# Performance work log

Hardware: AMD Instinct MI355X
Metric: run time of the kernel (lower is better)

The kernel has to match this reference:

```python
import jax, jax.numpy as jnp
import numpy as np

B, T, I, H = 8192, 1024, 3, 4


def setup_inputs() -> dict:
    key = jax.random.key(0)
    k_x, k_wi, k_wh, k_bi, k_bh = jax.random.split(key, 5)
    s = 1.0 / np.sqrt(H)  # PyTorch GRU init scale uniform(-1/sqrt(H), 1/sqrt(H))
    return {
        "x": jax.random.normal(k_x, (B, T, I), dtype=jnp.float32),
        "w_ih": jax.random.uniform(k_wi, (3 * H, I), jnp.float32, -s, s),
        "w_hh": jax.random.uniform(k_wh, (3 * H, H), jnp.float32, -s, s),
        "b_ih": jax.random.uniform(k_bi, (3 * H,), jnp.float32, -s, s),
        "b_hh": jax.random.uniform(k_bh, (3 * H,), jnp.float32, -s, s),
    }


def _gru_forward(x, w_ih, w_hh, b_ih, b_hh):
    # Precompute input projections for all timesteps: [B, T, 3H]
    gi = jnp.einsum('bti,gi->btg', x, w_ih) + b_ih
    gi = jnp.swapaxes(gi, 0, 1)  # [T, B, 3H] for scan over time
    h0 = jnp.zeros((x.shape[0], H), dtype=x.dtype)

    def step(h, gi_t):
        gh = h @ w_hh.T + b_hh                      # [B, 3H]
        i_r, i_z, i_n = jnp.split(gi_t, 3, axis=-1)
        h_r, h_z, h_n = jnp.split(gh, 3, axis=-1)
        r = jax.nn.sigmoid(i_r + h_r)
        z = jax.nn.sigmoid(i_z + h_z)
        n = jnp.tanh(i_n + r * h_n)
        h_new = (1.0 - z) * n + z * h
        return h_new, h_new

    h_last, outs = jax.lax.scan(step, h0, gi)
    out = jnp.swapaxes(outs, 0, 1)  # [B, T, H] (batch_first)
    h_n = h_last[None]              # [1, B, H] (num_layers*dirs, B, H)
    return out, h_n


def reference(x, w_ih, w_hh, b_ih, b_hh):
    return _gru_forward(x, w_ih, w_hh, b_ih, b_hh)
```

## Files before the change

kernel.cpp:

```cpp
#include <hip/hip_runtime.h>


#define TC 32
#define XS_STRIDE 99
#define OS_STRIDE 132

template<int CTRL>
__device__ __forceinline__ float dpp_rot(float v) {
    int i = __builtin_bit_cast(int, v);
    int r = __builtin_amdgcn_mov_dpp(i, CTRL, 0xf, 0xf, true);
    return __builtin_bit_cast(float, r);
}

__device__ __forceinline__ float vrcp(float x) { return __builtin_amdgcn_rcpf(x); }

__device__ __forceinline__ float sigmoid_f(float x) {
    return vrcp(1.0f + __expf(-x));
}
__device__ __forceinline__ float tanh_f(float x) {
    float e = __expf(2.0f * x);
    return 1.0f - 2.0f * vrcp(e + 1.0f);
}

__global__ __launch_bounds__(64) void gru_kernel(
    const float* __restrict__ x,
    const float* __restrict__ w_ih,
    const float* __restrict__ w_hh,
    const float* __restrict__ b_ih,
    const float* __restrict__ b_hh,
    float* __restrict__ out)
{
    __shared__ float x_s[16 * XS_STRIDE];
    __shared__ float out_s[16 * OS_STRIDE];

    const int lane = threadIdx.x;
    const int bl   = lane >> 2;
    const int j    = lane & 3;
    const int b0   = blockIdx.x * 16;

    float wir[3], wiz[3], win[3];
    #pragma unroll
    for (int k = 0; k < 3; ++k) {
        wir[k] = w_ih[j * 3 + k];
        wiz[k] = w_ih[(4 + j) * 3 + k];
        win[k] = w_ih[(8 + j) * 3 + k];
    }
    float whr[4], whz[4], whn[4];
    #pragma unroll
    for (int m = 0; m < 4; ++m) {
        int k = (j + m) & 3;
        whr[m] = w_hh[j * 4 + k];
        whz[m] = w_hh[(4 + j) * 4 + k];
        whn[m] = w_hh[(8 + j) * 4 + k];
    }
    const float br  = b_ih[j]     + b_hh[j];
    const float bz  = b_ih[4 + j] + b_hh[4 + j];
    const float bin = b_ih[8 + j];
    const float bhn = b_hh[8 + j];

    float h = 0.0f;

    float4 xr[6];
    {
        #pragma unroll
        for (int u = 0; u < 6; ++u) {
            int f  = u * 64 + lane;
            int bb = f / 24;
            int q  = f - bb * 24;
            xr[u] = *(const float4*)(x + (long long)(b0 + bb) * 3072 + q * 4);
        }
    }

    for (int c = 0; c < 32; ++c) {
        #pragma unroll
        for (int u = 0; u < 6; ++u) {
            int f  = u * 64 + lane;
            int bb = f / 24;
            int q  = f - bb * 24;
            float* p = &x_s[bb * XS_STRIDE + q * 4];
            p[0] = xr[u].x; p[1] = xr[u].y; p[2] = xr[u].z; p[3] = xr[u].w;
        }
        __syncthreads();

        if (c < 31) {
            int t0 = (c + 1) * TC;
            #pragma unroll
            for (int u = 0; u < 6; ++u) {
                int f  = u * 64 + lane;
                int bb = f / 24;
                int q  = f - bb * 24;
                xr[u] = *(const float4*)(x + (long long)(b0 + bb) * 3072 + t0 * 3 + q * 4);
            }
        }

        const float* xs = &x_s[bl * XS_STRIDE];
        float*       os = &out_s[bl * OS_STRIDE];
        #pragma unroll 8
        for (int t = 0; t < TC; ++t) {
            float x0 = xs[t * 3 + 0], x1 = xs[t * 3 + 1], x2 = xs[t * 3 + 2];
            float sr = fmaf(wir[0], x0, fmaf(wir[1], x1, fmaf(wir[2], x2, br)));
            float sz = fmaf(wiz[0], x0, fmaf(wiz[1], x1, fmaf(wiz[2], x2, bz)));
            float sn = fmaf(win[0], x0, fmaf(win[1], x1, fmaf(win[2], x2, bin)));

            float h1 = dpp_rot<0x39>(h);
            float h2 = dpp_rot<0x4E>(h);
            float h3 = dpp_rot<0x93>(h);

            float gr = fmaf(whr[0], h, fmaf(whr[1], h1, fmaf(whr[2], h2, whr[3] * h3)));
            float gz = fmaf(whz[0], h, fmaf(whz[1], h1, fmaf(whz[2], h2, whz[3] * h3)));
            float gn = fmaf(whn[0], h, fmaf(whn[1], h1, fmaf(whn[2], h2, whn[3] * h3)));

            float r = sigmoid_f(sr + gr);
            float z = sigmoid_f(sz + gz);
            float n = tanh_f(fmaf(r, gn + bhn, sn));
            h = fmaf(z, h - n, n);

            os[t * 4 + j] = h;
        }
        __syncthreads();

        int t0 = c * TC;
        #pragma unroll
        for (int u = 0; u < 8; ++u) {
            int f  = u * 64 + lane;
            int bb = f >> 5;
            int q  = f & 31;
            float4 v = *(const float4*)&out_s[bb * OS_STRIDE + q * 4];
            *(float4*)(out + (long long)(b0 + bb) * 4096 + t0 * 4 + q * 4) = v;
        }
    }

    out[33554432LL + (long long)(b0 + bl) * 4 + j] = h;
}

extern "C" void kernel_launch(void* const* d_in, const int* in_sizes, int n_in,
                              void* d_out, int out_size, void* d_ws, size_t ws_size,
                              hipStream_t stream) {
    const float* x    = (const float*)d_in[0];
    const float* w_ih = (const float*)d_in[1];
    const float* w_hh = (const float*)d_in[2];
    const float* b_ih = (const float*)d_in[3];
    const float* b_hh = (const float*)d_in[4];
    float* out = (float*)d_out;

    dim3 grid(512), block(64);
    gru_kernel<<<grid, block, 0, stream>>>(x, w_ih, w_hh, b_ih, b_hh, out);
}
```

Before: 278.6 us.

## Interleave two batch recurrences per wave and fold log2e into weights

Each 64-lane block now processes 32 batch rows instead of 16. Every lane advances two independent GRU chains interleaved per timestep, exposing instruction-level parallelism in the serial recurrence. Weights and biases are pre-scaled by -log2(e) or 2·log2(e) so the gate activations use raw exp2 and reciprocal with no extra multiplies. The grid is halved to 256 blocks, which may leave SIMDs idle and increase register and LDS use per block.

```diff
diff --git a/kernel.cpp b/kernel.cpp
--- a/kernel.cpp
+++ b/kernel.cpp
@@ -12,15 +12,8 @@
     return __builtin_bit_cast(float, r);
 }
 
-__device__ __forceinline__ float vrcp(float x) { return __builtin_amdgcn_rcpf(x); }
-
-__device__ __forceinline__ float sigmoid_f(float x) {
-    return vrcp(1.0f + __expf(-x));
-}
-__device__ __forceinline__ float tanh_f(float x) {
-    float e = __expf(2.0f * x);
-    return 1.0f - 2.0f * vrcp(e + 1.0f);
-}
+__device__ __forceinline__ float vrcp(float x)  { return __builtin_amdgcn_rcpf(x); }
+__device__ __forceinline__ float vexp2(float x) { return __builtin_amdgcn_exp2f(x); }
 
 __global__ __launch_bounds__(64) void gru_kernel(
     const float* __restrict__ x,
@@ -30,54 +23,55 @@
     const float* __restrict__ b_hh,
     float* __restrict__ out)
 {
-    __shared__ float x_s[16 * XS_STRIDE];
-    __shared__ float out_s[16 * OS_STRIDE];
+    __shared__ float x_s[32 * XS_STRIDE];
+    __shared__ float out_s[32 * OS_STRIDE];
 
     const int lane = threadIdx.x;
-    const int bl   = lane >> 2;
+    const int q    = lane >> 2;
     const int j    = lane & 3;
-    const int b0   = blockIdx.x * 16;
+    const int b0   = blockIdx.x * 32;
+
+    const float NL2E = -1.4426950408889634f;
+    const float P2   =  2.8853900817779268f;
 
     float wir[3], wiz[3], win[3];
     #pragma unroll
     for (int k = 0; k < 3; ++k) {
-        wir[k] = w_ih[j * 3 + k];
-        wiz[k] = w_ih[(4 + j) * 3 + k];
-        win[k] = w_ih[(8 + j) * 3 + k];
+        wir[k] = NL2E * w_ih[j * 3 + k];
+        wiz[k] = NL2E * w_ih[(4 + j) * 3 + k];
+        win[k] = P2   * w_ih[(8 + j) * 3 + k];
     }
     float whr[4], whz[4], whn[4];
     #pragma unroll
     for (int m = 0; m < 4; ++m) {
         int k = (j + m) & 3;
-        whr[m] = w_hh[j * 4 + k];
-        whz[m] = w_hh[(4 + j) * 4 + k];
-        whn[m] = w_hh[(8 + j) * 4 + k];
+        whr[m] = NL2E * w_hh[j * 4 + k];
+        whz[m] = NL2E * w_hh[(4 + j) * 4 + k];
+        whn[m] = P2   * w_hh[(8 + j) * 4 + k];
     }
-    const float br  = b_ih[j]     + b_hh[j];
-    const float bz  = b_ih[4 + j] + b_hh[4 + j];
-    const float bin = b_ih[8 + j];
-    const float bhn = b_hh[8 + j];
+    const float br   = NL2E * (b_ih[j]     + b_hh[j]);
+    const float bz   = NL2E * (b_ih[4 + j] + b_hh[4 + j]);
+    const float bin  = P2   * b_ih[8 + j];
+    const float bhn  = P2   * b_hh[8 + j];
 
-    float h = 0.0f;
+    float h[2] = {0.0f, 0.0f};
 
-    float4 xr[6];
-    {
-        #pragma unroll
-        for (int u = 0; u < 6; ++u) {
-            int f  = u * 64 + lane;
-            int bb = f / 24;
-            int q  = f - bb * 24;
-            xr[u] = *(const float4*)(x + (long long)(b0 + bb) * 3072 + q * 4);
-        }
+    float4 xr[12];
+    #pragma unroll
+    for (int u = 0; u < 12; ++u) {
+        int f  = u * 64 + lane;
+        int bb = f / 24;
+        int q4 = f - bb * 24;
+        xr[u] = *(const float4*)(x + (long long)(b0 + bb) * 3072 + q4 * 4);
     }
 
     for (int c = 0; c < 32; ++c) {
         #pragma unroll
-        for (int u = 0; u < 6; ++u) {
+        for (int u = 0; u < 12; ++u) {
             int f  = u * 64 + lane;
             int bb = f / 24;
-            int q  = f - bb * 24;
-            float* p = &x_s[bb * XS_STRIDE + q * 4];
+            int q4 = f - bb * 24;
+            float* p = &x_s[bb * XS_STRIDE + q4 * 4];
             p[0] = xr[u].x; p[1] = xr[u].y; p[2] = xr[u].z; p[3] = xr[u].w;
         }
         __syncthreads();
@@ -85,52 +79,63 @@
         if (c < 31) {
             int t0 = (c + 1) * TC;
             #pragma unroll
-            for (int u = 0; u < 6; ++u) {
+            for (int u = 0; u < 12; ++u) {
                 int f  = u * 64 + lane;
                 int bb = f / 24;
-                int q  = f - bb * 24;
-                xr[u] = *(const float4*)(x + (long long)(b0 + bb) * 3072 + t0 * 3 + q * 4);
+                int q4 = f - bb * 24;
+                xr[u] = *(const float4*)(x + (long long)(b0 + bb) * 3072 + t0 * 3 + q4 * 4);
             }
         }
 
-        const float* xs = &x_s[bl * XS_STRIDE];
-        float*       os = &out_s[bl * OS_STRIDE];
+        const float* xsA = &x_s[q * XS_STRIDE];
+        const float* xsB = &x_s[(q + 16) * XS_STRIDE];
+        float*       osA = &out_s[q * OS_STRIDE];
+        float*       osB = &out_s[(q + 16) * OS_STRIDE];
         #pragma unroll 8
         for (int t = 0; t < TC; ++t) {
-            float x0 = xs[t * 3 + 0], x1 = xs[t * 3 + 1], x2 = xs[t * 3 + 2];
-            float sr = fmaf(wir[0], x0, fmaf(wir[1], x1, fmaf(wir[2], x2, br)));
-            float sz = fmaf(wiz[0], x0, fmaf(wiz[1], x1, fmaf(wiz[2], x2, bz)));
-            float sn = fmaf(win[0], x0, fmaf(win[1], x1, fmaf(win[2], x2, bin)));
+            float x0[2], x1[2], x2[2];
+            x0[0] = xsA[t * 3 + 0]; x1[0] = xsA[t * 3 + 1]; x2[0] = xsA[t * 3 + 2];
+            x0[1] = xsB[t * 3 + 0]; x1[1] = xsB[t * 3 + 1]; x2[1] = xsB[t * 3 + 2];
+            #pragma unroll
+            for (int p = 0; p < 2; ++p) {
+                float sr = fmaf(wir[0], x0[p], fmaf(wir[1], x1[p], fmaf(wir[2], x2[p], br)));
+                float sz = fmaf(wiz[0], x0[p], fmaf(wiz[1], x1[p], fmaf(wiz[2], x2[p], bz)));
+                float sn = fmaf(win[0], x0[p], fmaf(win[1], x1[p], fmaf(win[2], x2[p], bin)));
 
-            float h1 = dpp_rot<0x39>(h);
-            float h2 = dpp_rot<0x4E>(h);
-            float h3 = dpp_rot<0x93>(h);
+                float h1 = dpp_rot<0x39>(h[p]);
+                float h2 = dpp_rot<0x4E>(h[p]);
+                float h3 = dpp_rot<0x93>(h[p]);
 
-            float gr = fmaf(whr[0], h, fmaf(whr[1], h1, fmaf(whr[2], h2, whr[3] * h3)));
-            float gz = fmaf(whz[0], h, fmaf(whz[1], h1, fmaf(whz[2], h2, whz[3] * h3)));
-            float gn = fmaf(whn[0], h, fmaf(whn[1], h1, fmaf(whn[2], h2, whn[3] * h3)));
+                float gr = fmaf(whr[0], h[p], fmaf(whr[1], h1, fmaf(whr[2], h2, whr[3] * h3)));
+                float gz = fmaf(whz[0], h[p], fmaf(whz[1], h1, fmaf(whz[2], h2, whz[3] * h3)));
+                float gn = fmaf(whn[0], h[p], fmaf(whn[1], h1, fmaf(whn[2], h2,
+                                 fmaf(whn[3], h3, bhn))));
 
-            float r = sigmoid_f(sr + gr);
-            float z = sigmoid_f(sz + gz);
-            float n = tanh_f(fmaf(r, gn + bhn, sn));
-            h = fmaf(z, h - n, n);
+                float r = vrcp(1.0f + vexp2(sr + gr));
+                float z = vrcp(1.0f + vexp2(sz + gz));
+                float an = fmaf(r, gn, sn);
+                float n  = fmaf(-2.0f, vrcp(1.0f + vexp2(an)), 1.0f);
 
-            os[t * 4 + j] = h;
+                h[p] = fmaf(z, h[p] - n, n);
+
+                (p == 0 ? osA : osB)[t * 4 + j] = h[p];
+            }
         }
         __syncthreads();
 
         int t0 = c * TC;
         #pragma unroll
-        for (int u = 0; u < 8; ++u) {
+        for (int u = 0; u < 16; ++u) {
             int f  = u * 64 + lane;
             int bb = f >> 5;
-            int q  = f & 31;
-            float4 v = *(const float4*)&out_s[bb * OS_STRIDE + q * 4];
-            *(float4*)(out + (long long)(b0 + bb) * 4096 + t0 * 4 + q * 4) = v;
+            int qq = f & 31;
+            float4 v = *(const float4*)&out_s[bb * OS_STRIDE + qq * 4];
+            *(float4*)(out + (long long)(b0 + bb) * 4096 + t0 * 4 + qq * 4) = v;
         }
     }
 
-    out[33554432LL + (long long)(b0 + bl) * 4 + j] = h;
+    out[33554432LL + (long long)(b0 + q) * 4 + j]      = h[0];
+    out[33554432LL + (long long)(b0 + 16 + q) * 4 + j] = h[1];
 }
 
 extern "C" void kernel_launch(void* const* d_in, const int* in_sizes, int n_in,
@@ -143,6 +148,6 @@
     const float* b_hh = (const float*)d_in[4];
     float* out = (float*)d_out;
 
-    dim3 grid(512), block(64);
+    dim3 grid(256), block(64);
     gru_kernel<<<grid, block, 0, stream>>>(x, w_ih, w_hh, b_ih, b_hh, out);
 }
```

Result: slower. 366.7 us (+31.6%).
